# Kernel optimization log

Hardware: AMD Instinct MI355X
Metric: run time of the kernel (lower is better)

The kernel has to match this reference:

```python
import jax, jax.numpy as jnp
import numpy as np

N, IN_F, OUT_F = 4096, 512, 256
GRAPH_DENSITY = 0.01
NEG_FILL = -1e11  # torch code uses -100000000000.0


def _normalise(g, remove_diagonal):
    # dense branch of normalise_graph (self_connection=False)
    if remove_diagonal:
        g = g - jnp.diag(jnp.diag(g))
    s = g.sum(axis=1)
    s = jnp.where(s == 0.0, 1.0, s)
    d = s ** -0.5
    return d[:, None] * g * d[None, :]


def setup_inputs() -> dict:
    key = jax.random.key(0)
    k1, k2, k3, k4, k5 = jax.random.split(key, 5)
    x = jax.random.normal(k1, (N, IN_F), jnp.float32)
    graph = (jax.random.uniform(k2, (N, N)) < GRAPH_DENSITY).astype(jnp.float32)
    # fc/weight: kaiming-normal-like init
    weight = jax.random.normal(k3, (OUT_F, IN_F), jnp.float32) * np.float32(np.sqrt(2.0 / IN_F))
    t_s = jax.random.normal(k4, (1, OUT_F), jnp.float32) * 0.05
    t_r = jax.random.normal(k5, (1, OUT_F), jnp.float32) * 0.05
    return {"x": x, "graph": graph, "weight": weight, "t_s": t_s, "t_r": t_r}


def reference(x, graph, weight, t_s, t_r):
    # H_ = input @ weight.T   (no bias, no dropout)
    H = x @ weight.T  # [N, OUT_F]

    # get_mask(graph, power=1): normalise(remove_diag) then normalise again
    mask = _normalise(_normalise(graph, remove_diagonal=True), remove_diagonal=False)  # [N, N]

    # get_edge_index_attention, dense path, attention_features == 1
    C1 = jax.nn.leaky_relu(H @ t_s.T, negative_slope=0.2)       # [N, 1]
    C2 = jax.nn.leaky_relu(H @ t_r.T, negative_slope=0.2).T    # [1, N]
    S = (mask * C1 + mask * C2) * 0.5                           # [N, N]
    S = jnp.where(mask <= 0.0, NEG_FILL, S)
    A = jax.nn.softmax(S, axis=1)                               # neighbourhood softmax

    # normalise_graph(A, remove_diagonal=False, self_connection=True), dense path
    A = A + jnp.eye(A.shape[0], dtype=A.dtype)
    s = A.sum(axis=1)
    s = jnp.where(s == 0.0, 1.0, s)
    d = s ** -0.5
    C = d[:, None] * A * d[None, :]

    return C @ H  # [N, OUT_F]
```

## Files before the change

kernel.cpp:

```cpp
#include <hip/hip_runtime.h>
#include <hip/hip_bf16.h>
#include <math.h>

#define N 4096
#define IN_F 512
#define OUT_F 256
#define CAP 128

typedef __attribute__((ext_vector_type(8))) short short8;
typedef __attribute__((ext_vector_type(4))) float float4v;

static __device__ __forceinline__ ushort f2bf(float f) {
  unsigned u = __float_as_uint(f);
  unsigned rnd = 0x7fffu + ((u >> 16) & 1u);
  return (ushort)((u + rnd) >> 16);
}
static __device__ __forceinline__ float bf2f(ushort us) {
  return __uint_as_float(((unsigned)us) << 16);
}

__global__ __launch_bounds__(256) void build_csr(
    const float* __restrict__ g, int* __restrict__ cols,
    int* __restrict__ deg, float* __restrict__ d1, float* __restrict__ c2r) {
  int i = blockIdx.x;
  __shared__ int s_cnt;
  if (threadIdx.x == 0) { s_cnt = 0; c2r[i] = 0.f; }
  __syncthreads();
  const float4* row4 = (const float4*)(g + (size_t)i * N);
  int lane = threadIdx.x & 63;
  for (int it = threadIdx.x; it < N / 4; it += 256) {
    float4 v = row4[it];
    int jb = it * 4;
    bool nz0 = (v.x != 0.f) && (jb + 0 != i);
    bool nz1 = (v.y != 0.f) && (jb + 1 != i);
    bool nz2 = (v.z != 0.f) && (jb + 2 != i);
    bool nz3 = (v.w != 0.f) && (jb + 3 != i);
    unsigned long long m0 = __ballot(nz0);
    unsigned long long m1 = __ballot(nz1);
    unsigned long long m2 = __ballot(nz2);
    unsigned long long m3 = __ballot(nz3);
    int p0 = __popcll(m0), p1 = __popcll(m1), p2 = __popcll(m2), p3 = __popcll(m3);
    int total = p0 + p1 + p2 + p3;
    if (total > 0) {
      int base;
      if (lane == 0) base = atomicAdd(&s_cnt, total);
      base = __shfl(base, 0);
      unsigned long long ltm = (1ull << lane) - 1ull;
      if (nz0) { int p = base + __popcll(m0 & ltm);                 if (p < CAP) cols[(size_t)i * CAP + p] = jb + 0; }
      if (nz1) { int p = base + p0 + __popcll(m1 & ltm);            if (p < CAP) cols[(size_t)i * CAP + p] = jb + 1; }
      if (nz2) { int p = base + p0 + p1 + __popcll(m2 & ltm);       if (p < CAP) cols[(size_t)i * CAP + p] = jb + 2; }
      if (nz3) { int p = base + p0 + p1 + p2 + __popcll(m3 & ltm);  if (p < CAP) cols[(size_t)i * CAP + p] = jb + 3; }
    }
  }
  __syncthreads();
  if (threadIdx.x == 0) {
    int c = s_cnt;
    deg[i] = (c > CAP) ? CAP : c;
    d1[i] = (c == 0) ? 1.f : rsqrtf((float)c);
  }
}

#define LDST 72
__global__ __launch_bounds__(256) void gemm_fused(
    const float* __restrict__ x, const float* __restrict__ wgt,
    const float* __restrict__ tr,
    const int* __restrict__ cols, const int* __restrict__ deg,
    const float* __restrict__ d1, float* __restrict__ w,
    float* __restrict__ H, ushort* __restrict__ Hb, float* __restrict__ c2r) {
  int bid = blockIdx.x;
  if (bid >= 256) {
    int wv = threadIdx.x >> 6, lane = threadIdx.x & 63;
    int wave_id = (bid - 256) * 4 + wv;
    for (int r = 0; r < 16; ++r) {
      int i = wave_id * 16 + r;
      int dgi = deg[i];
      float v = 0.f;
      if (lane < dgi)      v  = d1[cols[(size_t)i * CAP + lane]];
      if (lane + 64 < dgi) v += d1[cols[(size_t)i * CAP + lane + 64]];
      #pragma unroll
      for (int off = 32; off > 0; off >>= 1) v += __shfl_xor(v, off);
      if (lane == 0) {
        float s2 = d1[i] * v;
        w[i] = d1[i] * ((s2 == 0.f) ? 1.f : rsqrtf(s2));
      }
    }
    return;
  }
  __shared__ __align__(16) ushort As[64 * LDST];
  __shared__ __align__(16) ushort Bs[64 * LDST];
  int bm = (bid >> 2) * 64;
  int bn = (bid & 3) * 64;
  int tid = threadIdx.x;
  int lane = tid & 63;
  int wv = tid >> 6;
  int wm = (wv >> 1) * 32, wn = (wv & 1) * 32;

  float4v acc[2][2] = {{{0.f,0.f,0.f,0.f},{0.f,0.f,0.f,0.f}},
                       {{0.f,0.f,0.f,0.f},{0.f,0.f,0.f,0.f}}};

  for (int k0 = 0; k0 < IN_F; k0 += 64) {
    #pragma unroll
    for (int p = 0; p < 4; ++p) {
      int idx = p * 256 + tid;
      int row = idx >> 4;
      int cg = idx & 15;
      float4 va = *(const float4*)(x   + (size_t)(bm + row) * IN_F + k0 + cg * 4);
      float4 vb = *(const float4*)(wgt + (size_t)(bn + row) * IN_F + k0 + cg * 4);
      ushort4 pa, pb;
      pa.x = f2bf(va.x); pa.y = f2bf(va.y); pa.z = f2bf(va.z); pa.w = f2bf(va.w);
      pb.x = f2bf(vb.x); pb.y = f2bf(vb.y); pb.z = f2bf(vb.z); pb.w = f2bf(vb.w);
      *(ushort4*)(As + row * LDST + cg * 4) = pa;
      *(ushort4*)(Bs + row * LDST + cg * 4) = pb;
    }
    __syncthreads();
    #pragma unroll
    for (int kk = 0; kk < 64; kk += 32) {
      int kof = kk + (lane >> 4) * 8;
      short8 a0 = *(const short8*)(As + (wm +      (lane & 15)) * LDST + kof);
      short8 a1 = *(const short8*)(As + (wm + 16 + (lane & 15)) * LDST + kof);
      short8 b0 = *(const short8*)(Bs + (wn +      (lane & 15)) * LDST + kof);
      short8 b1 = *(const short8*)(Bs + (wn + 16 + (lane & 15)) * LDST + kof);
      acc[0][0] = __builtin_amdgcn_mfma_f32_16x16x32_bf16(a0, b0, acc[0][0], 0, 0, 0);
      acc[0][1] = __builtin_amdgcn_mfma_f32_16x16x32_bf16(a0, b1, acc[0][1], 0, 0, 0);
      acc[1][0] = __builtin_amdgcn_mfma_f32_16x16x32_bf16(a1, b0, acc[1][0], 0, 0, 0);
      acc[1][1] = __builtin_amdgcn_mfma_f32_16x16x32_bf16(a1, b1, acc[1][1], 0, 0, 0);
    }
    __syncthreads();
  }
  int ccol = lane & 15;
  int crow = (lane >> 4) * 4;
  float tr0 = tr[bn + wn + ccol], tr1 = tr[bn + wn + 16 + ccol];
  #pragma unroll
  for (int rt = 0; rt < 2; ++rt) {
    #pragma unroll
    for (int r = 0; r < 4; ++r) {
      float pr = acc[rt][0][r] * tr0 + acc[rt][1][r] * tr1;
      #pragma unroll
      for (int off = 1; off < 16; off <<= 1) pr += __shfl_xor(pr, off);
      if (ccol == 0) {
        int row = bm + wm + rt * 16 + crow + r;
        atomicAdd(&c2r[row], pr);
      }
    }
  }
  #pragma unroll
  for (int rt = 0; rt < 2; ++rt)
    #pragma unroll
    for (int ct = 0; ct < 2; ++ct)
      #pragma unroll
      for (int r = 0; r < 4; ++r) {
        int gr = bm + wm + rt * 16 + crow + r;
        int gc = bn + wn + ct * 16 + ccol;
        float v = acc[rt][ct][r];
        H[(size_t)gr * OUT_F + gc] = v;
        Hb[(size_t)gr * OUT_F + gc] = f2bf(v);
      }
}

__global__ __launch_bounds__(256) void aggregate(
    const float* __restrict__ H, const ushort* __restrict__ Hb,
    const int* __restrict__ cols, const int* __restrict__ deg,
    const float* __restrict__ w, const float* __restrict__ ts,
    const float* __restrict__ c2r, float* __restrict__ out) {
  __shared__ int sJ[4][CAP];
  __shared__ float sA[4][CAP];
  int wv = threadIdx.x >> 6;
  int lane = threadIdx.x & 63;
  int i = blockIdx.x * 4 + wv;
  int dgi = deg[i];
  float wi = w[i];

  float4 hself = ((const float4*)(H + (size_t)i * OUT_F))[lane];
  float4 t4 = ((const float4*)ts)[lane];
  float c1 = hself.x * t4.x + hself.y * t4.y + hself.z * t4.z + hself.w * t4.w;
  #pragma unroll
  for (int off = 32; off > 0; off >>= 1) c1 += __shfl_xor(c1, off);
  float ci = c1 > 0.f ? c1 : 0.2f * c1;

  float S0 = -1e30f, S1 = -1e30f;
  int j0 = 0, j1 = 0;
  if (lane < dgi) {
    j0 = cols[(size_t)i * CAP + lane];
    float c2v = c2r[j0];
    float cj = c2v > 0.f ? c2v : 0.2f * c2v;
    S0 = 0.5f * wi * w[j0] * (ci + cj);
  }
  if (lane + 64 < dgi) {
    j1 = cols[(size_t)i * CAP + lane + 64];
    float c2v = c2r[j1];
    float cj = c2v > 0.f ? c2v : 0.2f * c2v;
    S1 = 0.5f * wi * w[j1] * (ci + cj);
  }
  float mx = fmaxf(S0, S1);
  #pragma unroll
  for (int off = 32; off > 0; off >>= 1) mx = fmaxf(mx, __shfl_xor(mx, off));
  float e0 = (lane < dgi) ? __expf(S0 - mx) : 0.f;
  float e1 = (lane + 64 < dgi) ? __expf(S1 - mx) : 0.f;
  float Z = e0 + e1;
  #pragma unroll
  for (int off = 32; off > 0; off >>= 1) Z += __shfl_xor(Z, off);
  float half_invZ = 0.5f / Z;
  if (lane < dgi)      { sJ[wv][lane] = j0;        sA[wv][lane] = e0 * half_invZ; }
  if (lane + 64 < dgi) { sJ[wv][lane + 64] = j1;   sA[wv][lane + 64] = e1 * half_invZ; }

  float4 accv;
  accv.x = 0.5f * hself.x; accv.y = 0.5f * hself.y;
  accv.z = 0.5f * hself.z; accv.w = 0.5f * hself.w;

  if (dgi > 0) {
    int k = 0;
    for (; k + 8 <= dgi; k += 8) {
      int jj[8]; float aa[8];
      #pragma unroll
      for (int u = 0; u < 8; ++u) { jj[u] = sJ[wv][k + u]; aa[u] = sA[wv][k + u]; }
      ushort4 hb[8];
      #pragma unroll
      for (int u = 0; u < 8; ++u)
        hb[u] = ((const ushort4*)(Hb + (size_t)jj[u] * OUT_F))[lane];
      #pragma unroll
      for (int u = 0; u < 8; ++u) {
        accv.x += aa[u] * bf2f(hb[u].x);
        accv.y += aa[u] * bf2f(hb[u].y);
        accv.z += aa[u] * bf2f(hb[u].z);
        accv.w += aa[u] * bf2f(hb[u].w);
      }
    }
    for (; k < dgi; ++k) {
      int ja = sJ[wv][k];
      float aa = sA[wv][k];
      ushort4 hbv = ((const ushort4*)(Hb + (size_t)ja * OUT_F))[lane];
      accv.x += aa * bf2f(hbv.x); accv.y += aa * bf2f(hbv.y);
      accv.z += aa * bf2f(hbv.z); accv.w += aa * bf2f(hbv.w);
    }
  } else {
    float4 s = {0.f, 0.f, 0.f, 0.f};
    for (int r = 0; r < N; ++r) {
      ushort4 hbv = ((const ushort4*)(Hb + (size_t)r * OUT_F))[lane];
      s.x += bf2f(hbv.x); s.y += bf2f(hbv.y);
      s.z += bf2f(hbv.z); s.w += bf2f(hbv.w);
    }
    const float inv = 0.5f / (float)N;
    accv.x += s.x * inv; accv.y += s.y * inv;
    accv.z += s.z * inv; accv.w += s.w * inv;
  }
  ((float4*)(out + (size_t)i * OUT_F))[lane] = accv;
}

extern "C" void kernel_launch(void* const* d_in, const int* in_sizes, int n_in,
                              void* d_out, int out_size, void* d_ws, size_t ws_size,
                              hipStream_t stream) {
  const float* x     = (const float*)d_in[0];
  const float* graph = (const float*)d_in[1];
  const float* wgt   = (const float*)d_in[2];
  const float* ts    = (const float*)d_in[3];
  const float* tr    = (const float*)d_in[4];
  float* out = (float*)d_out;

  char* ws = (char*)d_ws;
  float*  H    = (float*) (ws);
  ushort* Hb   = (ushort*)(ws + (size_t)4 * 1024 * 1024);
  int*    cols = (int*)   (ws + (size_t)6 * 1024 * 1024);
  int*    deg  = (int*)   (ws + (size_t)8 * 1024 * 1024);
  float*  d1   = (float*) (ws + (size_t)8 * 1024 * 1024 + 16384);
  float*  w    = (float*) (ws + (size_t)8 * 1024 * 1024 + 32768);
  float*  c2r  = (float*) (ws + (size_t)8 * 1024 * 1024 + 49152);

  build_csr<<<N, 256, 0, stream>>>(graph, cols, deg, d1, c2r);
  gemm_fused<<<320, 256, 0, stream>>>(x, wgt, tr, cols, deg, d1, w, H, Hb, c2r);
  aggregate<<<N / 4, 256, 0, stream>>>(H, Hb, cols, deg, w, ts, c2r, out);
}
```

Before: 135.3 us.

## Fuse CSR build, GEMM and aggregation into one cooperative kernel with grid syncs

Replaces three kernel launches with a single cooperative kernel of 512 blocks that separates the phases with grid.sync(). The CSR build now gives one wave per row and uses a register counter instead of a shared-memory atomic per block. The degree-weight work runs on the spare blocks (256 and up) alongside the GEMM, and aggregation handles two rows per wave. This removes launch gaps and inter-kernel idle time, at the cost of grid-wide barrier overhead and fewer waves for the 16MB graph scan.

```diff
diff --git a/kernel.cpp b/kernel.cpp
--- a/kernel.cpp
+++ b/kernel.cpp
@@ -1,11 +1,14 @@
 #include <hip/hip_runtime.h>
-#include <hip/hip_bf16.h>
+#include <hip/hip_cooperative_groups.h>
 #include <math.h>
+
+namespace cg = cooperative_groups;
 
 #define N 4096
 #define IN_F 512
 #define OUT_F 256
 #define CAP 128
+#define LDST 72
 
 typedef __attribute__((ext_vector_type(8))) short short8;
 typedef __attribute__((ext_vector_type(4))) float float4v;
@@ -19,60 +22,127 @@
   return __uint_as_float(((unsigned)us) << 16);
 }
 
-__global__ __launch_bounds__(256) void build_csr(
-    const float* __restrict__ g, int* __restrict__ cols,
-    int* __restrict__ deg, float* __restrict__ d1, float* __restrict__ c2r) {
-  int i = blockIdx.x;
-  __shared__ int s_cnt;
-  if (threadIdx.x == 0) { s_cnt = 0; c2r[i] = 0.f; }
-  __syncthreads();
-  const float4* row4 = (const float4*)(g + (size_t)i * N);
-  int lane = threadIdx.x & 63;
-  for (int it = threadIdx.x; it < N / 4; it += 256) {
-    float4 v = row4[it];
-    int jb = it * 4;
-    bool nz0 = (v.x != 0.f) && (jb + 0 != i);
-    bool nz1 = (v.y != 0.f) && (jb + 1 != i);
-    bool nz2 = (v.z != 0.f) && (jb + 2 != i);
-    bool nz3 = (v.w != 0.f) && (jb + 3 != i);
-    unsigned long long m0 = __ballot(nz0);
-    unsigned long long m1 = __ballot(nz1);
-    unsigned long long m2 = __ballot(nz2);
-    unsigned long long m3 = __ballot(nz3);
-    int p0 = __popcll(m0), p1 = __popcll(m1), p2 = __popcll(m2), p3 = __popcll(m3);
-    int total = p0 + p1 + p2 + p3;
-    if (total > 0) {
-      int base;
-      if (lane == 0) base = atomicAdd(&s_cnt, total);
-      base = __shfl(base, 0);
-      unsigned long long ltm = (1ull << lane) - 1ull;
-      if (nz0) { int p = base + __popcll(m0 & ltm);                 if (p < CAP) cols[(size_t)i * CAP + p] = jb + 0; }
-      if (nz1) { int p = base + p0 + __popcll(m1 & ltm);            if (p < CAP) cols[(size_t)i * CAP + p] = jb + 1; }
-      if (nz2) { int p = base + p0 + p1 + __popcll(m2 & ltm);       if (p < CAP) cols[(size_t)i * CAP + p] = jb + 2; }
-      if (nz3) { int p = base + p0 + p1 + p2 + __popcll(m3 & ltm);  if (p < CAP) cols[(size_t)i * CAP + p] = jb + 3; }
+__global__ __launch_bounds__(256, 2) void mega(
+    const float* __restrict__ x, const float* __restrict__ g,
+    const float* __restrict__ wgt, const float* __restrict__ ts,
+    const float* __restrict__ tr, int* __restrict__ cols,
+    int* __restrict__ deg, float* __restrict__ d1, float* __restrict__ w,
+    float* __restrict__ c2r, float* __restrict__ H, ushort* __restrict__ Hb,
+    float* __restrict__ out) {
+  cg::grid_group grid = cg::this_grid();
+  __shared__ __align__(16) ushort smem[2 * 64 * LDST];
+  const int tid = threadIdx.x;
+  const int lane = tid & 63;
+  const int wv = tid >> 6;
+  const int bid = blockIdx.x;
+
+  #pragma unroll
+  for (int rr = 0; rr < 2; ++rr) {
+    int i = bid * 8 + rr * 4 + wv;
+    const float4* row4 = (const float4*)(g + (size_t)i * N);
+    int cnt = 0;
+    for (int it0 = 0; it0 < 16; it0 += 4) {
+      float4 v[4];
+      #pragma unroll
+      for (int u = 0; u < 4; ++u) v[u] = row4[(it0 + u) * 64 + lane];
+      #pragma unroll
+      for (int u = 0; u < 4; ++u) {
+        int jb = ((it0 + u) * 64 + lane) * 4;
+        bool nz0 = (v[u].x != 0.f) && (jb + 0 != i);
+        bool nz1 = (v[u].y != 0.f) && (jb + 1 != i);
+        bool nz2 = (v[u].z != 0.f) && (jb + 2 != i);
+        bool nz3 = (v[u].w != 0.f) && (jb + 3 != i);
+        unsigned long long m0 = __ballot(nz0), m1 = __ballot(nz1);
+        unsigned long long m2 = __ballot(nz2), m3 = __ballot(nz3);
+        int p0 = __popcll(m0), p1 = __popcll(m1), p2 = __popcll(m2), p3 = __popcll(m3);
+        unsigned long long ltm = (1ull << lane) - 1ull;
+        if (nz0) { int p = cnt + __popcll(m0 & ltm);                if (p < CAP) cols[(size_t)i * CAP + p] = jb + 0; }
+        if (nz1) { int p = cnt + p0 + __popcll(m1 & ltm);           if (p < CAP) cols[(size_t)i * CAP + p] = jb + 1; }
+        if (nz2) { int p = cnt + p0 + p1 + __popcll(m2 & ltm);      if (p < CAP) cols[(size_t)i * CAP + p] = jb + 2; }
+        if (nz3) { int p = cnt + p0 + p1 + p2 + __popcll(m3 & ltm); if (p < CAP) cols[(size_t)i * CAP + p] = jb + 3; }
+        cnt += p0 + p1 + p2 + p3;
+      }
+    }
+    if (lane == 0) {
+      deg[i] = (cnt > CAP) ? CAP : cnt;
+      d1[i] = cnt ? rsqrtf((float)cnt) : 1.f;
+      c2r[i] = 0.f;
     }
   }
-  __syncthreads();
-  if (threadIdx.x == 0) {
-    int c = s_cnt;
-    deg[i] = (c > CAP) ? CAP : c;
-    d1[i] = (c == 0) ? 1.f : rsqrtf((float)c);
-  }
-}
-
-#define LDST 72
-__global__ __launch_bounds__(256) void gemm_fused(
-    const float* __restrict__ x, const float* __restrict__ wgt,
-    const float* __restrict__ tr,
-    const int* __restrict__ cols, const int* __restrict__ deg,
-    const float* __restrict__ d1, float* __restrict__ w,
-    float* __restrict__ H, ushort* __restrict__ Hb, float* __restrict__ c2r) {
-  int bid = blockIdx.x;
-  if (bid >= 256) {
-    int wv = threadIdx.x >> 6, lane = threadIdx.x & 63;
-    int wave_id = (bid - 256) * 4 + wv;
-    for (int r = 0; r < 16; ++r) {
-      int i = wave_id * 16 + r;
+  grid.sync();
+
+  if (bid < 256) {
+    ushort* As = smem;
+    ushort* Bs = smem + 64 * LDST;
+    int bm = (bid >> 2) * 64;
+    int bn = (bid & 3) * 64;
+    int wm = (wv >> 1) * 32, wn = (wv & 1) * 32;
+
+    float4v acc[2][2] = {{{0.f,0.f,0.f,0.f},{0.f,0.f,0.f,0.f}},
+                         {{0.f,0.f,0.f,0.f},{0.f,0.f,0.f,0.f}}};
+
+    for (int k0 = 0; k0 < IN_F; k0 += 64) {
+      #pragma unroll
+      for (int p = 0; p < 4; ++p) {
+        int idx = p * 256 + tid;
+        int row = idx >> 4;
+        int cg4 = idx & 15;
+        float4 va = *(const float4*)(x   + (size_t)(bm + row) * IN_F + k0 + cg4 * 4);
+        float4 vb = *(const float4*)(wgt + (size_t)(bn + row) * IN_F + k0 + cg4 * 4);
+        ushort4 pa, pb;
+        pa.x = f2bf(va.x); pa.y = f2bf(va.y); pa.z = f2bf(va.z); pa.w = f2bf(va.w);
+        pb.x = f2bf(vb.x); pb.y = f2bf(vb.y); pb.z = f2bf(vb.z); pb.w = f2bf(vb.w);
+        *(ushort4*)(As + row * LDST + cg4 * 4) = pa;
+        *(ushort4*)(Bs + row * LDST + cg4 * 4) = pb;
+      }
+      __syncthreads();
+      #pragma unroll
+      for (int kk = 0; kk < 64; kk += 32) {
+        int kof = kk + (lane >> 4) * 8;
+        short8 a0 = *(const short8*)(As + (wm +      (lane & 15)) * LDST + kof);
+        short8 a1 = *(const short8*)(As + (wm + 16 + (lane & 15)) * LDST + kof);
+        short8 b0 = *(const short8*)(Bs + (wn +      (lane & 15)) * LDST + kof);
+        short8 b1 = *(const short8*)(Bs + (wn + 16 + (lane & 15)) * LDST + kof);
+        acc[0][0] = __builtin_amdgcn_mfma_f32_16x16x32_bf16(a0, b0, acc[0][0], 0, 0, 0);
+        acc[0][1] = __builtin_amdgcn_mfma_f32_16x16x32_bf16(a0, b1, acc[0][1], 0, 0, 0);
+        acc[1][0] = __builtin_amdgcn_mfma_f32_16x16x32_bf16(a1, b0, acc[1][0], 0, 0, 0);
+        acc[1][1] = __builtin_amdgcn_mfma_f32_16x16x32_bf16(a1, b1, acc[1][1], 0, 0, 0);
+      }
+      __syncthreads();
+    }
+    int ccol = lane & 15;
+    int crow = (lane >> 4) * 4;
+    float tr0 = tr[bn + wn + ccol], tr1 = tr[bn + wn + 16 + ccol];
+    #pragma unroll
+    for (int rt = 0; rt < 2; ++rt) {
+      #pragma unroll
+      for (int r = 0; r < 4; ++r) {
+        float pr = acc[rt][0][r] * tr0 + acc[rt][1][r] * tr1;
+        #pragma unroll
+        for (int off = 1; off < 16; off <<= 1) pr += __shfl_xor(pr, off);
+        if (ccol == 0) {
+          int row = bm + wm + rt * 16 + crow + r;
+          atomicAdd(&c2r[row], pr);
+        }
+      }
+    }
+    #pragma unroll
+    for (int rt = 0; rt < 2; ++rt)
+      #pragma unroll
+      for (int ct = 0; ct < 2; ++ct)
+        #pragma unroll
+        for (int r = 0; r < 4; ++r) {
+          int gr = bm + wm + rt * 16 + crow + r;
+          int gc = bn + wn + ct * 16 + ccol;
+          float v = acc[rt][ct][r];
+          H[(size_t)gr * OUT_F + gc] = v;
+          Hb[(size_t)gr * OUT_F + gc] = f2bf(v);
+        }
+  } else {
+    int w_id = (bid - 256) * 4 + wv;
+    #pragma unroll
+    for (int r = 0; r < 4; ++r) {
+      int i = w_id * 4 + r;
       int dgi = deg[i];
       float v = 0.f;
       if (lane < dgi)      v  = d1[cols[(size_t)i * CAP + lane]];
@@ -84,166 +154,92 @@
         w[i] = d1[i] * ((s2 == 0.f) ? 1.f : rsqrtf(s2));
       }
     }
-    return;
   }
-  __shared__ __align__(16) ushort As[64 * LDST];
-  __shared__ __align__(16) ushort Bs[64 * LDST];
-  int bm = (bid >> 2) * 64;
-  int bn = (bid & 3) * 64;
-  int tid = threadIdx.x;
-  int lane = tid & 63;
-  int wv = tid >> 6;
-  int wm = (wv >> 1) * 32, wn = (wv & 1) * 32;
-
-  float4v acc[2][2] = {{{0.f,0.f,0.f,0.f},{0.f,0.f,0.f,0.f}},
-                       {{0.f,0.f,0.f,0.f},{0.f,0.f,0.f,0.f}}};
-
-  for (int k0 = 0; k0 < IN_F; k0 += 64) {
-    #pragma unroll
-    for (int p = 0; p < 4; ++p) {
-      int idx = p * 256 + tid;
-      int row = idx >> 4;
-      int cg = idx & 15;
-      float4 va = *(const float4*)(x   + (size_t)(bm + row) * IN_F + k0 + cg * 4);
-      float4 vb = *(const float4*)(wgt + (size_t)(bn + row) * IN_F + k0 + cg * 4);
-      ushort4 pa, pb;
-      pa.x = f2bf(va.x); pa.y = f2bf(va.y); pa.z = f2bf(va.z); pa.w = f2bf(va.w);
-      pb.x = f2bf(vb.x); pb.y = f2bf(vb.y); pb.z = f2bf(vb.z); pb.w = f2bf(vb.w);
-      *(ushort4*)(As + row * LDST + cg * 4) = pa;
-      *(ushort4*)(Bs + row * LDST + cg * 4) = pb;
-    }
-    __syncthreads();
-    #pragma unroll
-    for (int kk = 0; kk < 64; kk += 32) {
-      int kof = kk + (lane >> 4) * 8;
-      short8 a0 = *(const short8*)(As + (wm +      (lane & 15)) * LDST + kof);
-      short8 a1 = *(const short8*)(As + (wm + 16 + (lane & 15)) * LDST + kof);
-      short8 b0 = *(const short8*)(Bs + (wn +      (lane & 15)) * LDST + kof);
-      short8 b1 = *(const short8*)(Bs + (wn + 16 + (lane & 15)) * LDST + kof);
-      acc[0][0] = __builtin_amdgcn_mfma_f32_16x16x32_bf16(a0, b0, acc[0][0], 0, 0, 0);
-      acc[0][1] = __builtin_amdgcn_mfma_f32_16x16x32_bf16(a0, b1, acc[0][1], 0, 0, 0);
-      acc[1][0] = __builtin_amdgcn_mfma_f32_16x16x32_bf16(a1, b0, acc[1][0], 0, 0, 0);
-      acc[1][1] = __builtin_amdgcn_mfma_f32_16x16x32_bf16(a1, b1, acc[1][1], 0, 0, 0);
-    }
-    __syncthreads();
+  grid.sync();
+
+  int*   sJ = (int*)smem + wv * CAP;
+  float* sA = (float*)((char*)smem + 4 * CAP * 4) + wv * CAP;
+  #pragma unroll
+  for (int rr = 0; rr < 2; ++rr) {
+    int i = bid * 4 + wv + rr * 2048;
+    int dgi = deg[i];
+    float wi = w[i];
+
+    float4 hself = ((const float4*)(H + (size_t)i * OUT_F))[lane];
+    float4 t4 = ((const float4*)ts)[lane];
+    float c1 = hself.x * t4.x + hself.y * t4.y + hself.z * t4.z + hself.w * t4.w;
+    #pragma unroll
+    for (int off = 32; off > 0; off >>= 1) c1 += __shfl_xor(c1, off);
+    float ci = c1 > 0.f ? c1 : 0.2f * c1;
+
+    float S0 = -1e30f, S1 = -1e30f;
+    int j0 = 0, j1 = 0;
+    if (lane < dgi) {
+      j0 = cols[(size_t)i * CAP + lane];
+      float c2v = c2r[j0];
+      float cj = c2v > 0.f ? c2v : 0.2f * c2v;
+      S0 = 0.5f * wi * w[j0] * (ci + cj);
+    }
+    if (lane + 64 < dgi) {
+      j1 = cols[(size_t)i * CAP + lane + 64];
+      float c2v = c2r[j1];
+      float cj = c2v > 0.f ? c2v : 0.2f * c2v;
+      S1 = 0.5f * wi * w[j1] * (ci + cj);
+    }
+    float mx = fmaxf(S0, S1);
+    #pragma unroll
+    for (int off = 32; off > 0; off >>= 1) mx = fmaxf(mx, __shfl_xor(mx, off));
+    float e0 = (lane < dgi) ? __expf(S0 - mx) : 0.f;
+    float e1 = (lane + 64 < dgi) ? __expf(S1 - mx) : 0.f;
+    float Z = e0 + e1;
+    #pragma unroll
+    for (int off = 32; off > 0; off >>= 1) Z += __shfl_xor(Z, off);
+    float half_invZ = 0.5f / Z;
+    if (lane < dgi)      { sJ[lane] = j0;       sA[lane] = e0 * half_invZ; }
+    if (lane + 64 < dgi) { sJ[lane + 64] = j1;  sA[lane + 64] = e1 * half_invZ; }
+
+    float4 accv;
+    accv.x = 0.5f * hself.x; accv.y = 0.5f * hself.y;
+    accv.z = 0.5f * hself.z; accv.w = 0.5f * hself.w;
+
+    if (dgi > 0) {
+      int k = 0;
+      for (; k + 8 <= dgi; k += 8) {
+        int jj[8]; float aa[8];
+        #pragma unroll
+        for (int u = 0; u < 8; ++u) { jj[u] = sJ[k + u]; aa[u] = sA[k + u]; }
+        ushort4 hb[8];
+        #pragma unroll
+        for (int u = 0; u < 8; ++u)
+          hb[u] = ((const ushort4*)(Hb + (size_t)jj[u] * OUT_F))[lane];
+        #pragma unroll
+        for (int u = 0; u < 8; ++u) {
+          accv.x += aa[u] * bf2f(hb[u].x);
+          accv.y += aa[u] * bf2f(hb[u].y);
+          accv.z += aa[u] * bf2f(hb[u].z);
+          accv.w += aa[u] * bf2f(hb[u].w);
+        }
+      }
+      for (; k < dgi; ++k) {
+        int ja = sJ[k];
+        float aa = sA[k];
+        ushort4 hbv = ((const ushort4*)(Hb + (size_t)ja * OUT_F))[lane];
+        accv.x += aa * bf2f(hbv.x); accv.y += aa * bf2f(hbv.y);
+        accv.z += aa * bf2f(hbv.z); accv.w += aa * bf2f(hbv.w);
+      }
+    } else {
+      float4 s = {0.f, 0.f, 0.f, 0.f};
+      for (int r = 0; r < N; ++r) {
+        ushort4 hbv = ((const ushort4*)(Hb + (size_t)r * OUT_F))[lane];
+        s.x += bf2f(hbv.x); s.y += bf2f(hbv.y);
+        s.z += bf2f(hbv.z); s.w += bf2f(hbv.w);
+      }
+      const float inv = 0.5f / (float)N;
+      accv.x += s.x * inv; accv.y += s.y * inv;
+      accv.z += s.z * inv; accv.w += s.w * inv;
+    }
+    ((float4*)(out + (size_t)i * OUT_F))[lane] = accv;
   }
-  int ccol = lane & 15;
-  int crow = (lane >> 4) * 4;
-  float tr0 = tr[bn + wn + ccol], tr1 = tr[bn + wn + 16 + ccol];
-  #pragma unroll
-  for (int rt = 0; rt < 2; ++rt) {
-    #pragma unroll
-    for (int r = 0; r < 4; ++r) {
-      float pr = acc[rt][0][r] * tr0 + acc[rt][1][r] * tr1;
-      #pragma unroll
-      for (int off = 1; off < 16; off <<= 1) pr += __shfl_xor(pr, off);
-      if (ccol == 0) {
-        int row = bm + wm + rt * 16 + crow + r;
-        atomicAdd(&c2r[row], pr);
-      }
-    }
-  }
-  #pragma unroll
-  for (int rt = 0; rt < 2; ++rt)
-    #pragma unroll
-    for (int ct = 0; ct < 2; ++ct)
-      #pragma unroll
-      for (int r = 0; r < 4; ++r) {
-        int gr = bm + wm + rt * 16 + crow + r;
-        int gc = bn + wn + ct * 16 + ccol;
-        float v = acc[rt][ct][r];
-        H[(size_t)gr * OUT_F + gc] = v;
-        Hb[(size_t)gr * OUT_F + gc] = f2bf(v);
-      }
-}
-
-__global__ __launch_bounds__(256) void aggregate(
-    const float* __restrict__ H, const ushort* __restrict__ Hb,
-    const int* __restrict__ cols, const int* __restrict__ deg,
-    const float* __restrict__ w, const float* __restrict__ ts,
-    const float* __restrict__ c2r, float* __restrict__ out) {
-  __shared__ int sJ[4][CAP];
-  __shared__ float sA[4][CAP];
-  int wv = threadIdx.x >> 6;
-  int lane = threadIdx.x & 63;
-  int i = blockIdx.x * 4 + wv;
-  int dgi = deg[i];
-  float wi = w[i];
-
-  float4 hself = ((const float4*)(H + (size_t)i * OUT_F))[lane];
-  float4 t4 = ((const float4*)ts)[lane];
-  float c1 = hself.x * t4.x + hself.y * t4.y + hself.z * t4.z + hself.w * t4.w;
-  #pragma unroll
-  for (int off = 32; off > 0; off >>= 1) c1 += __shfl_xor(c1, off);
-  float ci = c1 > 0.f ? c1 : 0.2f * c1;
-
-  float S0 = -1e30f, S1 = -1e30f;
-  int j0 = 0, j1 = 0;
-  if (lane < dgi) {
-    j0 = cols[(size_t)i * CAP + lane];
-    float c2v = c2r[j0];
-    float cj = c2v > 0.f ? c2v : 0.2f * c2v;
-    S0 = 0.5f * wi * w[j0] * (ci + cj);
-  }
-  if (lane + 64 < dgi) {
-    j1 = cols[(size_t)i * CAP + lane + 64];
-    float c2v = c2r[j1];
-    float cj = c2v > 0.f ? c2v : 0.2f * c2v;
-    S1 = 0.5f * wi * w[j1] * (ci + cj);
-  }
-  float mx = fmaxf(S0, S1);
-  #pragma unroll
-  for (int off = 32; off > 0; off >>= 1) mx = fmaxf(mx, __shfl_xor(mx, off));
-  float e0 = (lane < dgi) ? __expf(S0 - mx) : 0.f;
-  float e1 = (lane + 64 < dgi) ? __expf(S1 - mx) : 0.f;
-  float Z = e0 + e1;
-  #pragma unroll
-  for (int off = 32; off > 0; off >>= 1) Z += __shfl_xor(Z, off);
-  float half_invZ = 0.5f / Z;
-  if (lane < dgi)      { sJ[wv][lane] = j0;        sA[wv][lane] = e0 * half_invZ; }
-  if (lane + 64 < dgi) { sJ[wv][lane + 64] = j1;   sA[wv][lane + 64] = e1 * half_invZ; }
-
-  float4 accv;
-  accv.x = 0.5f * hself.x; accv.y = 0.5f * hself.y;
-  accv.z = 0.5f * hself.z; accv.w = 0.5f * hself.w;
-
-  if (dgi > 0) {
-    int k = 0;
-    for (; k + 8 <= dgi; k += 8) {
-      int jj[8]; float aa[8];
-      #pragma unroll
-      for (int u = 0; u < 8; ++u) { jj[u] = sJ[wv][k + u]; aa[u] = sA[wv][k + u]; }
-      ushort4 hb[8];
-      #pragma unroll
-      for (int u = 0; u < 8; ++u)
-        hb[u] = ((const ushort4*)(Hb + (size_t)jj[u] * OUT_F))[lane];
-      #pragma unroll
-      for (int u = 0; u < 8; ++u) {
-        accv.x += aa[u] * bf2f(hb[u].x);
-        accv.y += aa[u] * bf2f(hb[u].y);
-        accv.z += aa[u] * bf2f(hb[u].z);
-        accv.w += aa[u] * bf2f(hb[u].w);
-      }
-    }
-    for (; k < dgi; ++k) {
-      int ja = sJ[wv][k];
-      float aa = sA[wv][k];
-      ushort4 hbv = ((const ushort4*)(Hb + (size_t)ja * OUT_F))[lane];
-      accv.x += aa * bf2f(hbv.x); accv.y += aa * bf2f(hbv.y);
-      accv.z += aa * bf2f(hbv.z); accv.w += aa * bf2f(hbv.w);
-    }
-  } else {
-    float4 s = {0.f, 0.f, 0.f, 0.f};
-    for (int r = 0; r < N; ++r) {
-      ushort4 hbv = ((const ushort4*)(Hb + (size_t)r * OUT_F))[lane];
-      s.x += bf2f(hbv.x); s.y += bf2f(hbv.y);
-      s.z += bf2f(hbv.z); s.w += bf2f(hbv.w);
-    }
-    const float inv = 0.5f / (float)N;
-    accv.x += s.x * inv; accv.y += s.y * inv;
-    accv.z += s.z * inv; accv.w += s.w * inv;
-  }
-  ((float4*)(out + (size_t)i * OUT_F))[lane] = accv;
 }
 
 extern "C" void kernel_launch(void* const* d_in, const int* in_sizes, int n_in,
@@ -265,7 +261,6 @@
   float*  w    = (float*) (ws + (size_t)8 * 1024 * 1024 + 32768);
   float*  c2r  = (float*) (ws + (size_t)8 * 1024 * 1024 + 49152);
 
-  build_csr<<<N, 256, 0, stream>>>(graph, cols, deg, d1, c2r);
-  gemm_fused<<<320, 256, 0, stream>>>(x, wgt, tr, cols, deg, d1, w, H, Hb, c2r);
-  aggregate<<<N / 4, 256, 0, stream>>>(H, Hb, cols, deg, w, ts, c2r, out);
-}
+  void* args[] = {&x, &graph, &wgt, &ts, &tr, &cols, &deg, &d1, &w, &c2r, &H, &Hb, &out};
+  hipLaunchCooperativeKernel((const void*)mega, dim3(512), dim3(256), args, 0, stream);
+}
```

Measured after the change: 277.0 us. +104.7%, slower.
